# Performance work log

Hardware: AMD Instinct MI355X
Metric: run time of the kernel (lower is better)

## Reference

```python
import jax, jax.numpy as jnp
import numpy as np

EPS = 1e-5


def _rmsnorm(x, eps=EPS):
    return x * jax.lax.rsqrt(jnp.mean(x * x, axis=-1, keepdims=True) + eps)


def _bitlinear(x, w):
    # fla-style BitLinear: RMSNorm (no affine) -> 8-bit activation quant (STE)
    # -> ternary weight quant (STE) -> linear. w is [out, in].
    xn = _rmsnorm(x)
    s = 127.0 / jnp.clip(jnp.max(jnp.abs(xn), axis=-1, keepdims=True), 1e-5, None)
    xq = jnp.clip(jnp.round(xn * s), -128.0, 127.0) / s
    xq = xn + jax.lax.stop_gradient(xq - xn)
    ws = 1.0 / jnp.clip(jnp.mean(jnp.abs(w)), 1e-5, None)
    wq = jnp.clip(jnp.round(w * ws), -1.0, 1.0) / ws
    wq = w + jax.lax.stop_gradient(wq - w)
    return jnp.einsum('bld,od->blo', xq, wq)


def _hgrn_scan(i, f):
    # h_t = f_t * h_{t-1} + i_t along axis=2 (seq), h_0 = 0.
    def combine(a, b):
        fa, ia = a
        fb, ib = b
        return fa * fb, ia * fb + ib
    _, h = jax.lax.associative_scan(combine, (f, i), axis=2)
    return h


def _forward(hidden_states, Wi, Wf, Wg, Wo, g_norm_weight, num_heads=1):
    b, l, d = hidden_states.shape
    i = _bitlinear(hidden_states, Wi)
    f = jax.nn.sigmoid(_bitlinear(hidden_states, Wf))
    i = jax.nn.silu(i) * (1.0 - f)  # swiglu(i, 1-f)
    # [b, l, (h d)] -> [b, h, l, d_head]
    i = i.reshape(b, l, num_heads, -1).transpose(0, 2, 1, 3)
    f = f.reshape(b, l, num_heads, -1).transpose(0, 2, 1, 3)
    h = _hgrn_scan(i, f)
    h = h.transpose(0, 2, 1, 3).reshape(b, l, d)
    # FusedRMSNormSwishGate: rmsnorm(g)*weight * h*sigmoid(h)
    g = _bitlinear(hidden_states, Wg)
    o = _rmsnorm(g) * g_norm_weight * (h * jax.nn.sigmoid(h))
    return _bitlinear(o, Wo)


def setup_inputs() -> dict:
    key = jax.random.key(0)
    ks = jax.random.split(key, 5)
    B, L, D = 4, 2048, 2048
    gain = 2 ** (-2.5) * (6.0 / (2 * D)) ** 0.5  # xavier_uniform with gain 2^-2.5
    def w(k):
        return jax.random.uniform(k, (D, D), jnp.float32, -gain, gain)
    return {
        'hidden_states': jax.random.normal(ks[0], (B, L, D), jnp.float32),
        'Wi': w(ks[1]),
        'Wf': w(ks[2]),
        'Wg': w(ks[3]),
        'Wo': w(ks[4]),
        'g_norm_weight': jnp.ones((D,), jnp.float32),
    }


def reference(hidden_states, Wi, Wf, Wg, Wo, g_norm_weight):
    return _forward(hidden_states, Wi, Wf, Wg, Wo, g_norm_weight)
```

## Files before the change

kernel.cpp:

```cpp
#include <hip/hip_runtime.h>
#include <stdint.h>

#define B_DIM 4
#define L_DIM 2048
#define D_DIM 2048
#define M_DIM 8192
#define K_DIM 2048
#define N_DIM 2048
#define WELEM (D_DIM * D_DIM)
#define CHUNK 32
#define NCH (L_DIM / CHUNK)

typedef int v4i  __attribute__((ext_vector_type(4)));
typedef int v16i __attribute__((ext_vector_type(16)));
typedef unsigned short bfraw;

#define AS1 __attribute__((address_space(1)))
#define AS3 __attribute__((address_space(3)))

__device__ __forceinline__ void gl_lds16(const void* g, void* l) {
    __builtin_amdgcn_global_load_lds((AS1 void*)g, (AS3 void*)l, 16, 0, 0);
}

__device__ __forceinline__ void wg_barrier() {
    asm volatile("" ::: "memory");
    __builtin_amdgcn_s_barrier();
    asm volatile("" ::: "memory");
}

__device__ __forceinline__ float sigmoidf_(float x) { return 1.0f / (1.0f + expf(-x)); }

__device__ __forceinline__ float bf2f(bfraw u) {
    union { unsigned int i; float f; } c; c.i = ((unsigned int)u) << 16; return c.f;
}
__device__ __forceinline__ bfraw f2bf(float f) {
    union { float f; unsigned int i; } c; c.f = f;
    unsigned int lsb = (c.i >> 16) & 1;
    c.i += 0x7fffu + lsb;
    return (bfraw)(c.i >> 16);
}

__device__ __forceinline__ void store_out(float* p, float v) { *p = v; }
__device__ __forceinline__ void store_out(bfraw* p, float v) { *p = f2bf(v); }

__device__ __forceinline__ float block_sum256(float v) {
#pragma unroll
    for (int off = 32; off > 0; off >>= 1) v += __shfl_down(v, off);
    __shared__ float sb[4];
    int lane = threadIdx.x & 63, wv = threadIdx.x >> 6;
    __syncthreads();
    if (lane == 0) sb[wv] = v;
    __syncthreads();
    return sb[0] + sb[1] + sb[2] + sb[3];
}

__device__ __forceinline__ void block_sum_max256(float& s, float& m) {
#pragma unroll
    for (int off = 32; off > 0; off >>= 1) {
        s += __shfl_down(s, off);
        m = fmaxf(m, __shfl_down(m, off));
    }
    __shared__ float sb2[8];
    int lane = threadIdx.x & 63, wv = threadIdx.x >> 6;
    __syncthreads();
    if (lane == 0) { sb2[wv] = s; sb2[4 + wv] = m; }
    __syncthreads();
    s = sb2[0] + sb2[1] + sb2[2] + sb2[3];
    m = fmaxf(fmaxf(sb2[4], sb2[5]), fmaxf(sb2[6], sb2[7]));
}

__global__ void wstats1(const float* __restrict__ w0, const float* __restrict__ w1,
                        const float* __restrict__ w2, const float* __restrict__ w3,
                        float* __restrict__ wpart) {
    int w = blockIdx.x >> 7;
    int slice = blockIdx.x & 127;
    const float* W = (w == 0) ? w0 : ((w == 1) ? w1 : ((w == 2) ? w2 : w3));
    const float4* p = (const float4*)(W + (size_t)slice * (WELEM / 128));
    float s = 0.f;
    for (int i = threadIdx.x; i < (WELEM / 128 / 4); i += 256) {
        float4 v = p[i];
        s += fabsf(v.x) + fabsf(v.y) + fabsf(v.z) + fabsf(v.w);
    }
    s = block_sum256(s);
    if (threadIdx.x == 0) wpart[blockIdx.x] = s;
}

__global__ void wstats2(const float* __restrict__ wpart, float* __restrict__ wdeq) {
    int w = threadIdx.x >> 6;
    int lane = threadIdx.x & 63;
    float s = wpart[w * 128 + lane] + wpart[w * 128 + 64 + lane];
#pragma unroll
    for (int off = 32; off > 0; off >>= 1) s += __shfl_down(s, off);
    if (lane == 0) wdeq[w] = fmaxf(s * (1.0f / (float)WELEM), 1e-5f);
}

__global__ void quant_all(const float* __restrict__ w0, const float* __restrict__ w1,
                          const float* __restrict__ w2, const float* __restrict__ w3,
                          const float* __restrict__ wdeq, int8_t* __restrict__ wq,
                          const float* __restrict__ x, int8_t* __restrict__ xq,
                          float* __restrict__ adeq) {
    if (blockIdx.x < 16384) {
        size_t idx = (size_t)blockIdx.x * 256 + threadIdx.x;
        int w = (int)(idx >> 20);
        size_t g = idx & ((1u << 20) - 1);
        const float* W = (w == 0) ? w0 : ((w == 1) ? w1 : ((w == 2) ? w2 : w3));
        float inv = 1.0f / wdeq[w];
        float4 v = ((const float4*)W)[g];
        int q0 = (int)rintf(v.x * inv); q0 = q0 < -1 ? -1 : (q0 > 1 ? 1 : q0);
        int q1 = (int)rintf(v.y * inv); q1 = q1 < -1 ? -1 : (q1 > 1 ? 1 : q1);
        int q2 = (int)rintf(v.z * inv); q2 = q2 < -1 ? -1 : (q2 > 1 ? 1 : q2);
        int q3 = (int)rintf(v.w * inv); q3 = q3 < -1 ? -1 : (q3 > 1 ? 1 : q3);
        uint32_t p = (uint32_t)(q0 & 0xff) | ((uint32_t)(q1 & 0xff) << 8) |
                     ((uint32_t)(q2 & 0xff) << 16) | ((uint32_t)(q3 & 0xff) << 24);
        ((uint32_t*)(wq + (size_t)w * WELEM))[g] = p;
        return;
    }
    int row = blockIdx.x - 16384, tid = threadIdx.x;
    const float4* xr = (const float4*)(x + (size_t)row * D_DIM);
    float4 a = xr[2 * tid], b = xr[2 * tid + 1];
    float v[8] = {a.x, a.y, a.z, a.w, b.x, b.y, b.z, b.w};
    float ss = 0.f, mx = 0.f;
#pragma unroll
    for (int j = 0; j < 8; j++) { ss += v[j] * v[j]; mx = fmaxf(mx, fabsf(v[j])); }
    block_sum_max256(ss, mx);
    float inv = rsqrtf(ss * (1.0f / (float)D_DIM) + 1e-5f);
    float anc = fmaxf(mx * inv, 1e-5f);
    float s = 127.0f / anc;
    if (tid == 0) adeq[row] = anc * (1.0f / 127.0f);
    float sc = inv * s;
    int q[8];
#pragma unroll
    for (int j = 0; j < 8; j++) {
        int t = (int)rintf(v[j] * sc);
        q[j] = t < -128 ? -128 : (t > 127 ? 127 : t);
    }
    uint32_t lo = (uint32_t)(q[0] & 0xff) | ((uint32_t)(q[1] & 0xff) << 8) |
                  ((uint32_t)(q[2] & 0xff) << 16) | ((uint32_t)(q[3] & 0xff) << 24);
    uint32_t hi = (uint32_t)(q[4] & 0xff) | ((uint32_t)(q[5] & 0xff) << 8) |
                  ((uint32_t)(q[6] & 0xff) << 16) | ((uint32_t)(q[7] & 0xff) << 24);
    ((uint2*)(xq + (size_t)row * D_DIM))[tid] = make_uint2(lo, hi);
}

#define BM2 256
#define BN2 256
#define BKB 64
#define NT (K_DIM / BKB)

#define MFMA32(a, b, c) __builtin_amdgcn_mfma_i32_32x32x32_i8((a), (b), (c), 0, 0, 0)

template <typename OutT>
__device__ __forceinline__ void gemm_core(
    const int8_t* __restrict__ A, const int8_t* __restrict__ Bw,
    const float* __restrict__ adeq, float wsc,
    int m0, int n0, OutT* __restrict__ Cout) {
    __shared__ __align__(16) int8_t sA[3][BM2 * BKB];
    __shared__ __align__(16) int8_t sB[3][BN2 * BKB];
    int lane = threadIdx.x & 63;
    int wv = threadIdx.x >> 6;
    int wr = wv >> 2, wc = wv & 3;
    int r32 = lane & 31;
    int h32 = lane >> 5;
    const int ag = wr * 4;
    const int bg = wc * 2;
    const int lb = lane * 16;

    const v16i vzero = {0, 0, 0, 0, 0, 0, 0, 0, 0, 0, 0, 0, 0, 0, 0, 0};
    v16i acc[4][2];
#pragma unroll
    for (int m = 0; m < 4; m++)
#pragma unroll
        for (int n = 0; n < 2; n++) acc[m][n] = vzero;

    const int8_t* Asrc = A + (size_t)(m0 + r32) * K_DIM + h32 * 16;
    const int8_t* Bsrc = Bw + (size_t)(n0 + r32) * K_DIM + h32 * 16;

#define STG(c, kt, s) do {                                                                  \
    gl_lds16(Asrc + (size_t)(wv * 32) * K_DIM + (kt) + (s) * 32, &sA[c][wv * 2048 + (s) * 1024]); \
    gl_lds16(Bsrc + (size_t)(wv * 32) * K_DIM + (kt) + (s) * 32, &sB[c][wv * 2048 + (s) * 1024]); \
  } while (0)

#define LDF(buf, grp, s) (*(const v4i*)(&(buf)[(grp) * 2048 + (s) * 1024 + lb]))

    STG(0, 0, 0);   STG(0, 0, 1);
    STG(1, BKB, 0); STG(1, BKB, 1);
    asm volatile("s_waitcnt vmcnt(4)" ::: "memory");
    wg_barrier();

    int cur = 0;
    for (int t = 0; t < NT; ++t) {
        const int8_t* bA = &sA[cur][0];
        const int8_t* bB = &sB[cur][0];
        int c2 = cur + 2; if (c2 >= 3) c2 -= 3;
        int kt2 = (t + 2) * BKB;

        v4i a0s0 = LDF(bA, ag + 0, 0), a0s1 = LDF(bA, ag + 0, 1);
        v4i a1s0 = LDF(bA, ag + 1, 0), a1s1 = LDF(bA, ag + 1, 1);
        v4i b0s0 = LDF(bB, bg + 0, 0), b0s1 = LDF(bB, bg + 0, 1);
        v4i b1s0 = LDF(bB, bg + 1, 0), b1s1 = LDF(bB, bg + 1, 1);
        if (t + 2 < NT) STG(c2, kt2, 0);
        wg_barrier();
        asm volatile("s_waitcnt lgkmcnt(0)" ::: "memory");
        __builtin_amdgcn_sched_barrier(0);
        __builtin_amdgcn_s_setprio(1);
        acc[0][0] = MFMA32(a0s0, b0s0, acc[0][0]);
        acc[1][0] = MFMA32(a1s0, b0s0, acc[1][0]);
        acc[0][1] = MFMA32(a0s0, b1s0, acc[0][1]);
        acc[1][1] = MFMA32(a1s0, b1s0, acc[1][1]);
        acc[0][0] = MFMA32(a0s1, b0s1, acc[0][0]);
        acc[1][0] = MFMA32(a1s1, b0s1, acc[1][0]);
        acc[0][1] = MFMA32(a0s1, b1s1, acc[0][1]);
        acc[1][1] = MFMA32(a1s1, b1s1, acc[1][1]);
        __builtin_amdgcn_s_setprio(0);
        wg_barrier();

        v4i a2s0 = LDF(bA, ag + 2, 0), a2s1 = LDF(bA, ag + 2, 1);
        v4i a3s0 = LDF(bA, ag + 3, 0), a3s1 = LDF(bA, ag + 3, 1);
        if (t + 2 < NT) {
            STG(c2, kt2, 1);
            asm volatile("s_waitcnt vmcnt(4)" ::: "memory");
        } else if (t + 1 < NT) {
            asm volatile("s_waitcnt vmcnt(0)" ::: "memory");
        }
        wg_barrier();
        asm volatile("s_waitcnt lgkmcnt(0)" ::: "memory");
        __builtin_amdgcn_sched_barrier(0);
        __builtin_amdgcn_s_setprio(1);
        acc[2][0] = MFMA32(a2s0, b0s0, acc[2][0]);
        acc[3][0] = MFMA32(a3s0, b0s0, acc[3][0]);
        acc[2][1] = MFMA32(a2s0, b1s0, acc[2][1]);
        acc[3][1] = MFMA32(a3s0, b1s0, acc[3][1]);
        acc[2][0] = MFMA32(a2s1, b0s1, acc[2][0]);
        acc[3][0] = MFMA32(a3s1, b0s1, acc[3][0]);
        acc[2][1] = MFMA32(a2s1, b1s1, acc[2][1]);
        acc[3][1] = MFMA32(a3s1, b1s1, acc[3][1]);
        __builtin_amdgcn_s_setprio(0);
        wg_barrier();

        cur = cur + 1; if (cur >= 3) cur = 0;
    }
#undef LDF
#undef STG

#pragma unroll
    for (int m = 0; m < 4; m++) {
#pragma unroll
        for (int r = 0; r < 16; r++) {
            int rr = (r & 3) + 8 * (r >> 2) + 4 * h32;
            int row = m0 + (ag + m) * 32 + rr;
            float rs = adeq[row] * wsc;
            OutT* crow = Cout + (size_t)row * N_DIM + n0 + bg * 32 + r32;
            store_out(crow,      (float)acc[m][0][r] * rs);
            store_out(crow + 32, (float)acc[m][1][r] * rs);
        }
    }
}

__global__ __launch_bounds__(512, 2) void gemm_ifg(
    const int8_t* __restrict__ xq, const int8_t* __restrict__ wq,
    const float* __restrict__ adeq, const float* __restrict__ wdeq,
    bfraw* __restrict__ bufI, bfraw* __restrict__ bufF, bfraw* __restrict__ bufG) {
    int widx = blockIdx.x >> 3;
    int n0 = (blockIdx.x & 7) * BN2;
    int m0 = blockIdx.y * BM2;
    bfraw* outp = (widx == 0) ? bufI : ((widx == 1) ? bufF : bufG);
    gemm_core<bfraw>(xq, wq + (size_t)widx * WELEM, adeq, wdeq[widx], m0, n0, outp);
}

__global__ __launch_bounds__(512, 2) void gemm_o(
    const int8_t* __restrict__ oq, const int8_t* __restrict__ wq,
    const float* __restrict__ odeq, const float* __restrict__ wdeq,
    float* __restrict__ out) {
    gemm_core<float>(oq, wq + 3 * (size_t)WELEM, odeq, wdeq[3], blockIdx.y * BM2,
                     blockIdx.x * BN2, out);
}

__global__ void scan1(const bfraw* __restrict__ iL, const bfraw* __restrict__ fL,
                      float* __restrict__ Fc, float* __restrict__ Ic) {
    int idx = blockIdx.x * 256 + threadIdx.x;
    int d = idx & (D_DIM - 1);
    int c = (idx >> 11) & (NCH - 1);
    int b = idx >> 17;
    size_t base = ((size_t)(b * L_DIM + c * CHUNK)) * D_DIM + d;
    float F = 1.f, h = 0.f;
#pragma unroll 4
    for (int t = 0; t < CHUNK; t++) {
        float fr = bf2f(fL[base + (size_t)t * D_DIM]);
        float ir = bf2f(iL[base + (size_t)t * D_DIM]);
        float fv = sigmoidf_(fr);
        float iv = ir * sigmoidf_(ir) * (1.0f - fv);
        h = fv * h + iv;
        F *= fv;
    }
    size_t ci = ((size_t)b * NCH + c) * D_DIM + d;
    Fc[ci] = F;
    Ic[ci] = h;
}

__global__ void scan2(const float* __restrict__ Fc, const float* __restrict__ Ic,
                      float* __restrict__ Hc) {
    int idx = blockIdx.x * 256 + threadIdx.x;
    int d = idx & (D_DIM - 1);
    int b = idx >> 11;
    float h = 0.f;
    for (int c0 = 0; c0 < NCH; c0 += 8) {
        float F[8], I[8];
#pragma unroll
        for (int j = 0; j < 8; j++) {
            size_t ci = ((size_t)b * NCH + c0 + j) * D_DIM + d;
            F[j] = Fc[ci];
            I[j] = Ic[ci];
        }
#pragma unroll
        for (int j = 0; j < 8; j++) {
            size_t ci = ((size_t)b * NCH + c0 + j) * D_DIM + d;
            Hc[ci] = h;
            h = F[j] * h + I[j];
        }
    }
}

__global__ void scan3(const bfraw* __restrict__ iL, const bfraw* __restrict__ fL,
                      const float* __restrict__ Hc, bfraw* __restrict__ hout) {
    int idx = blockIdx.x * 256 + threadIdx.x;
    int d = idx & (D_DIM - 1);
    int c = (idx >> 11) & (NCH - 1);
    int b = idx >> 17;
    size_t base = ((size_t)(b * L_DIM + c * CHUNK)) * D_DIM + d;
    float h = Hc[((size_t)b * NCH + c) * D_DIM + d];
#pragma unroll 4
    for (int t = 0; t < CHUNK; t++) {
        size_t a = base + (size_t)t * D_DIM;
        float fr = bf2f(fL[a]);
        float ir = bf2f(iL[a]);
        float fv = sigmoidf_(fr);
        float iv = ir * sigmoidf_(ir) * (1.0f - fv);
        h = fv * h + iv;
        hout[a] = f2bf(h);
    }
}

union BF8 { uint4 u; bfraw s[8]; };

__global__ void gout_quant(const bfraw* __restrict__ gL, const bfraw* __restrict__ h,
                           const float* __restrict__ gw, int8_t* __restrict__ oq,
                           float* __restrict__ odeq) {
    int row = blockIdx.x, tid = threadIdx.x;
    BF8 g8, h8;
    g8.u = ((const uint4*)(gL + (size_t)row * D_DIM))[tid];
    float gv[8];
    float ss = 0.f;
#pragma unroll
    for (int j = 0; j < 8; j++) { gv[j] = bf2f(g8.s[j]); ss += gv[j] * gv[j]; }
    float ssg = block_sum256(ss);
    float invg = rsqrtf(ssg * (1.0f / (float)D_DIM) + 1e-5f);

    h8.u = ((const uint4*)(h + (size_t)row * D_DIM))[tid];
    const float4* wr = (const float4*)gw;
    float4 w0 = wr[2 * tid], w1 = wr[2 * tid + 1];
    float wv[8] = {w0.x, w0.y, w0.z, w0.w, w1.x, w1.y, w1.z, w1.w};
    float o[8];
    float sso = 0.f, amax = 0.f;
#pragma unroll
    for (int j = 0; j < 8; j++) {
        float hv = bf2f(h8.s[j]);
        o[j] = gv[j] * invg * wv[j] * hv * sigmoidf_(hv);
        sso += o[j] * o[j];
        amax = fmaxf(amax, fabsf(o[j]));
    }
    block_sum_max256(sso, amax);
    float invo = rsqrtf(sso * (1.0f / (float)D_DIM) + 1e-5f);
    float anc = fmaxf(amax * invo, 1e-5f);
    float s = 127.0f / anc;
    if (tid == 0) odeq[row] = anc * (1.0f / 127.0f);
    float sc = invo * s;
    int q[8];
#pragma unroll
    for (int j = 0; j < 8; j++) {
        int t = (int)rintf(o[j] * sc);
        q[j] = t < -128 ? -128 : (t > 127 ? 127 : t);
    }
    uint32_t lo = (uint32_t)(q[0] & 0xff) | ((uint32_t)(q[1] & 0xff) << 8) |
                  ((uint32_t)(q[2] & 0xff) << 16) | ((uint32_t)(q[3] & 0xff) << 24);
    uint32_t hi = (uint32_t)(q[4] & 0xff) | ((uint32_t)(q[5] & 0xff) << 8) |
                  ((uint32_t)(q[6] & 0xff) << 16) | ((uint32_t)(q[7] & 0xff) << 24);
    ((uint2*)(oq + (size_t)row * D_DIM))[tid] = make_uint2(lo, hi);
}

extern "C" void kernel_launch(void* const* d_in, const int* in_sizes, int n_in,
                              void* d_out, int out_size, void* d_ws, size_t ws_size,
                              hipStream_t stream) {
    const float* x  = (const float*)d_in[0];
    const float* Wi = (const float*)d_in[1];
    const float* Wf = (const float*)d_in[2];
    const float* Wg = (const float*)d_in[3];
    const float* Wo = (const float*)d_in[4];
    const float* gw = (const float*)d_in[5];
    float* out = (float*)d_out;

    char* ws = (char*)d_ws;
    float*  wdeq  = (float*)(ws + 0);
    float*  wpart = (float*)(ws + 256);
    float*  adeq  = (float*)(ws + 0x10000);
    float*  odeq  = (float*)(ws + 0x20000);
    int8_t* xq    = (int8_t*)(ws + 0x100000);
    int8_t* wq    = (int8_t*)(ws + 0x1100000);
    float*  Fc    = (float*)(ws + 0x2100000);
    float*  Ic    = (float*)(ws + 0x2300000);
    float*  Hc    = (float*)(ws + 0x2500000);
    bfraw*  bufI  = (bfraw*)(ws + 0x4000000);
    bfraw*  bufF  = (bfraw*)(ws + 0x6000000);
    bfraw*  bufG  = (bfraw*)(ws + 0x8000000);
    bfraw*  hbuf  = (bfraw*)(ws + 0xA000000);

    wstats1<<<512, 256, 0, stream>>>(Wi, Wf, Wg, Wo, wpart);
    wstats2<<<1, 256, 0, stream>>>(wpart, wdeq);
    quant_all<<<16384 + 8192, 256, 0, stream>>>(Wi, Wf, Wg, Wo, wdeq, wq, x, xq, adeq);

    gemm_ifg<<<dim3(24, M_DIM / BM2), 512, 0, stream>>>(xq, wq, adeq, wdeq, bufI, bufF, bufG);

    scan1<<<2048, 256, 0, stream>>>(bufI, bufF, Fc, Ic);
    scan2<<<32, 256, 0, stream>>>(Fc, Ic, Hc);
    scan3<<<2048, 256, 0, stream>>>(bufI, bufF, Hc, hbuf);

    gout_quant<<<M_DIM, 256, 0, stream>>>(bufG, hbuf, gw, xq , odeq);
    gemm_o<<<dim3(N_DIM / BN2, M_DIM / BM2), 512, 0, stream>>>(xq , wq, odeq, wdeq, out);

    (void)in_sizes; (void)n_in; (void)out_size; (void)ws_size;
}
```

Before: 454.7 us.

## Use 4-stage LDS ring with one barrier per K-tile in int8 GEMM

Result: faster. 418.7 us (-7.9%).

```diff
diff --git a/kernel.cpp b/kernel.cpp
--- a/kernel.cpp
+++ b/kernel.cpp
@@ -153,8 +153,8 @@
     const int8_t* __restrict__ A, const int8_t* __restrict__ Bw,
     const float* __restrict__ adeq, float wsc,
     int m0, int n0, OutT* __restrict__ Cout) {
-    __shared__ __align__(16) int8_t sA[3][BM2 * BKB];
-    __shared__ __align__(16) int8_t sB[3][BN2 * BKB];
+    __shared__ __align__(16) int8_t sA[4][BM2 * BKB];
+    __shared__ __align__(16) int8_t sB[4][BN2 * BKB];
     int lane = threadIdx.x & 63;
     int wv = threadIdx.x >> 6;
     int wr = wv >> 2, wc = wv & 3;
@@ -174,69 +174,56 @@
     const int8_t* Asrc = A + (size_t)(m0 + r32) * K_DIM + h32 * 16;
     const int8_t* Bsrc = Bw + (size_t)(n0 + r32) * K_DIM + h32 * 16;
 
-#define STG(c, kt, s) do {                                                                  \
-    gl_lds16(Asrc + (size_t)(wv * 32) * K_DIM + (kt) + (s) * 32, &sA[c][wv * 2048 + (s) * 1024]); \
-    gl_lds16(Bsrc + (size_t)(wv * 32) * K_DIM + (kt) + (s) * 32, &sB[c][wv * 2048 + (s) * 1024]); \
+#define STG(c, kt) do {                                                                     \
+    gl_lds16(Asrc + (size_t)(wv * 32) * K_DIM + (kt),      &sA[c][wv * 2048]);              \
+    gl_lds16(Asrc + (size_t)(wv * 32) * K_DIM + (kt) + 32, &sA[c][wv * 2048 + 1024]);       \
+    gl_lds16(Bsrc + (size_t)(wv * 32) * K_DIM + (kt),      &sB[c][wv * 2048]);              \
+    gl_lds16(Bsrc + (size_t)(wv * 32) * K_DIM + (kt) + 32, &sB[c][wv * 2048 + 1024]);       \
   } while (0)
 
 #define LDF(buf, grp, s) (*(const v4i*)(&(buf)[(grp) * 2048 + (s) * 1024 + lb]))
 
-    STG(0, 0, 0);   STG(0, 0, 1);
-    STG(1, BKB, 0); STG(1, BKB, 1);
+    STG(0, 0);
+    STG(1, BKB);
     asm volatile("s_waitcnt vmcnt(4)" ::: "memory");
     wg_barrier();
 
-    int cur = 0;
     for (int t = 0; t < NT; ++t) {
+        int cur = t & 3;
         const int8_t* bA = &sA[cur][0];
         const int8_t* bB = &sB[cur][0];
-        int c2 = cur + 2; if (c2 >= 3) c2 -= 3;
-        int kt2 = (t + 2) * BKB;
-
-        v4i a0s0 = LDF(bA, ag + 0, 0), a0s1 = LDF(bA, ag + 0, 1);
-        v4i a1s0 = LDF(bA, ag + 1, 0), a1s1 = LDF(bA, ag + 1, 1);
-        v4i b0s0 = LDF(bB, bg + 0, 0), b0s1 = LDF(bB, bg + 0, 1);
-        v4i b1s0 = LDF(bB, bg + 1, 0), b1s1 = LDF(bB, bg + 1, 1);
-        if (t + 2 < NT) STG(c2, kt2, 0);
-        wg_barrier();
-        asm volatile("s_waitcnt lgkmcnt(0)" ::: "memory");
-        __builtin_amdgcn_sched_barrier(0);
+
+        v4i af[4][2], bf[2][2];
+#pragma unroll
+        for (int m = 0; m < 4; m++) {
+            af[m][0] = LDF(bA, ag + m, 0);
+            af[m][1] = LDF(bA, ag + m, 1);
+        }
+#pragma unroll
+        for (int n = 0; n < 2; n++) {
+            bf[n][0] = LDF(bB, bg + n, 0);
+            bf[n][1] = LDF(bB, bg + n, 1);
+        }
+
+        if (t + 2 < NT) STG((t + 2) & 3, (t + 2) * BKB);
+
         __builtin_amdgcn_s_setprio(1);
-        acc[0][0] = MFMA32(a0s0, b0s0, acc[0][0]);
-        acc[1][0] = MFMA32(a1s0, b0s0, acc[1][0]);
-        acc[0][1] = MFMA32(a0s0, b1s0, acc[0][1]);
-        acc[1][1] = MFMA32(a1s0, b1s0, acc[1][1]);
-        acc[0][0] = MFMA32(a0s1, b0s1, acc[0][0]);
-        acc[1][0] = MFMA32(a1s1, b0s1, acc[1][0]);
-        acc[0][1] = MFMA32(a0s1, b1s1, acc[0][1]);
-        acc[1][1] = MFMA32(a1s1, b1s1, acc[1][1]);
+#pragma unroll
+        for (int s = 0; s < 2; s++)
+#pragma unroll
+            for (int m = 0; m < 4; m++)
+#pragma unroll
+                for (int n = 0; n < 2; n++)
+                    acc[m][n] = MFMA32(af[m][s], bf[n][s], acc[m][n]);
         __builtin_amdgcn_s_setprio(0);
-        wg_barrier();
-
-        v4i a2s0 = LDF(bA, ag + 2, 0), a2s1 = LDF(bA, ag + 2, 1);
-        v4i a3s0 = LDF(bA, ag + 3, 0), a3s1 = LDF(bA, ag + 3, 1);
-        if (t + 2 < NT) {
-            STG(c2, kt2, 1);
-            asm volatile("s_waitcnt vmcnt(4)" ::: "memory");
-        } else if (t + 1 < NT) {
-            asm volatile("s_waitcnt vmcnt(0)" ::: "memory");
-        }
-        wg_barrier();
-        asm volatile("s_waitcnt lgkmcnt(0)" ::: "memory");
-        __builtin_amdgcn_sched_barrier(0);
-        __builtin_amdgcn_s_setprio(1);
-        acc[2][0] = MFMA32(a2s0, b0s0, acc[2][0]);
-        acc[3][0] = MFMA32(a3s0, b0s0, acc[3][0]);
-        acc[2][1] = MFMA32(a2s0, b1s0, acc[2][1]);
-        acc[3][1] = MFMA32(a3s0, b1s0, acc[3][1]);
-        acc[2][0] = MFMA32(a2s1, b0s1, acc[2][0]);
-        acc[3][0] = MFMA32(a3s1, b0s1, acc[3][0]);
-        acc[2][1] = MFMA32(a2s1, b1s1, acc[2][1]);
-        acc[3][1] = MFMA32(a3s1, b1s1, acc[3][1]);
-        __builtin_amdgcn_s_setprio(0);
-        wg_barrier();
-
-        cur = cur + 1; if (cur >= 3) cur = 0;
+
+        if (t + 1 < NT) {
+            if (t + 2 < NT)
+                asm volatile("s_waitcnt vmcnt(4)" ::: "memory");
+            else
+                asm volatile("s_waitcnt vmcnt(0)" ::: "memory");
+            wg_barrier();
+        }
     }
 #undef LDF
 #undef STG
```
